# Kernel optimization log

Measured on AMD Instinct MI355X. Metric: run time of the kernel, lower is better.

The kernel has to match this reference:

```python
import jax, jax.numpy as jnp
import numpy as np

NN = 1024  # nodes per LSTM layer (equal across layers, required by gating broadcast)


def setup_inputs() -> dict:
    key = jax.random.key(0)
    ks = jax.random.split(key, 8)
    T, B, V, E = 64, 64, 32000, 512
    ip = 0.3
    inputs = jax.random.normal(ks[0], (T, B, V), dtype=jnp.float32) * 0.1
    embedding_matrix = jax.random.normal(ks[1], (V, E), dtype=jnp.float32) * (ip * np.sqrt(1.0 / V))
    lstm_w0 = jax.random.normal(ks[2], (E + NN, 4 * NN), dtype=jnp.float32) * (ip * np.sqrt(1.0 / (E + NN)))
    lstm_b0 = jnp.zeros((4 * NN,), dtype=jnp.float32)
    lstm_w1 = jax.random.normal(ks[3], (2 * NN, 4 * NN), dtype=jnp.float32) * (ip * np.sqrt(1.0 / (2 * NN)))
    lstm_b1 = jnp.zeros((4 * NN,), dtype=jnp.float32)
    gates_w = jax.random.normal(ks[4], (2 * NN, 2), dtype=jnp.float32) * (ip * np.sqrt(1.0 / (2 * NN)))
    out_w = jax.random.normal(ks[5], (NN, V), dtype=jnp.float32) * (ip * np.sqrt(1.0 / NN))
    out_b = jnp.zeros((V,), dtype=jnp.float32)
    return dict(inputs=inputs, embedding_matrix=embedding_matrix,
                lstm_w0=lstm_w0, lstm_b0=lstm_b0, lstm_w1=lstm_w1, lstm_b1=lstm_b1,
                gates_w=gates_w, out_w=out_w, out_b=out_b)


def _cell(x, h, c, W, b):
    # concat -> matmul -> bias -> split [3*NN sigmoid | NN tanh] -> gate update
    z = jnp.concatenate([x, h], axis=1) @ W + b
    sig = jax.nn.sigmoid(z[:, : 3 * NN])
    g = jnp.tanh(z[:, 3 * NN:])
    f, i, o = sig[:, :NN], sig[:, NN:2 * NN], sig[:, 2 * NN:]
    c_new = f * c + i * g
    h_new = o * jnp.tanh(c_new)
    return h_new, c_new


def _forward(inputs, embedding_matrix, lstm_w0, lstm_b0, lstm_w1, lstm_b1, gates_w, out_w, out_b):
    T, B, V = inputs.shape
    emb = jnp.einsum('tbv,ve->tbe', inputs, embedding_matrix)  # [T,B,E]

    def step(carry, e_t):
        h0, c0, h1, c1 = carry
        h0, c0 = _cell(e_t, h0, c0, lstm_w0, lstm_b0)
        h1, c1 = _cell(h0, h1, c1, lstm_w1, lstm_b1)
        return (h0, c0, h1, c1), (h0, h1)

    zeros = jnp.zeros((B, NN), dtype=inputs.dtype)
    _, (h0s, h1s) = jax.lax.scan(step, (zeros, zeros, zeros, zeros), emb)
    h0_flat = h0s.reshape(T * B, NN)  # concat along time == stacked reshape
    h1_flat = h1s.reshape(T * B, NN)
    full = jnp.concatenate([h0_flat, h1_flat], axis=1)  # [T*B, 2*NN]
    gates = jax.nn.sigmoid(full @ gates_w)               # [T*B, 2]
    gated = gates[:, 0:1] * h0_flat + gates[:, 1:2] * h1_flat
    logits = gated @ out_w + out_b                       # [T*B, V]
    return logits


def reference(inputs, embedding_matrix, lstm_w0, lstm_b0, lstm_w1, lstm_b1, gates_w, out_w, out_b):
    return _forward(inputs, embedding_matrix, lstm_w0, lstm_b0, lstm_w1, lstm_b1, gates_w, out_w, out_b)
```

## Files before the change

kernel.cpp:

```cpp
#include <hip/hip_runtime.h>
#include <math.h>

typedef __attribute__((ext_vector_type(8))) short bf16x8;
typedef __attribute__((ext_vector_type(4))) float f32x4;
typedef __attribute__((ext_vector_type(8))) _Float16 f16x8;
typedef unsigned short ushort_t;

#define T_STEPS 64
#define BATCH   64
#define VOCAB   32000
#define EMB     512
#define HID     1024
#define G4      4096

__device__ __forceinline__ unsigned short f2bf(float x) {
    unsigned u = __builtin_bit_cast(unsigned, x);
    u += 0x7FFFu + ((u >> 16) & 1u);
    return (unsigned short)(u >> 16);
}
__device__ __forceinline__ float bf2f(unsigned short h) {
    unsigned u = ((unsigned)h) << 16;
    return __builtin_bit_cast(float, u);
}
__device__ __forceinline__ unsigned pack2(unsigned short a, unsigned short b) {
    return (unsigned)a | ((unsigned)b << 16);
}
__device__ __forceinline__ unsigned short f2h(float x) {
    return __builtin_bit_cast(unsigned short, (_Float16)x);
}
__device__ __forceinline__ float h2f(unsigned short h) {
    return (float)__builtin_bit_cast(_Float16, h);
}
__device__ __forceinline__ f32x4 ntload4(const float* p) {
    return __builtin_nontemporal_load((const f32x4*)p);
}

__device__ __forceinline__ size_t packA_off(int row, int k, int M16) {
    return ((size_t)((k >> 5) * M16 + (row >> 4))) * 512 +
           ((k & 31) >> 3) * 128 + (row & 15) * 8 + (k & 7);
}

template<int BM, int BN, int NW_M, int NW_N, bool NTA, bool NTC>
__launch_bounds__(NW_M * NW_N * 64)
__global__ void gemm_a32b16(const float* __restrict__ A, const ushort_t* __restrict__ Bp,
                            float* __restrict__ C, int lda, int ldc, int K8,
                            int KCHUNK, size_t chunkStride, float invScale) {
    constexpr int THREADS = NW_M * NW_N * 64;
    constexpr int MF = BM / NW_M / 16;
    constexpr int NF = BN / NW_N / 16;
    __shared__ _Float16 AhS[BM][40];

    const int tid  = threadIdx.x;
    const int row0 = blockIdx.y * BM;
    const int gBase = blockIdx.x * (BN / 16);
    const int kBeg = blockIdx.z * KCHUNK;
    C += (size_t)blockIdx.z * chunkStride;

    const int l = tid & 63, w = tid >> 6;
    const int wm = w / NW_N, wn = w % NW_N;
    const int lr = l & 15, lk = l >> 4;

    f32x4 acc[MF][NF];
#pragma unroll
    for (int m = 0; m < MF; ++m)
#pragma unroll
        for (int n = 0; n < NF; ++n)
#pragma unroll
            for (int r = 0; r < 4; ++r) acc[m][n][r] = 0.f;

    constexpr int AI = BM * 4 / THREADS;

    for (int k0 = 0; k0 < KCHUNK; k0 += 32) {
#pragma unroll
        for (int i = 0; i < AI; ++i) {
            int f = tid + i * THREADS;
            int r = f >> 2, k8 = (f & 3) << 3;
            const float* ap = A + (size_t)(row0 + r) * lda + kBeg + k0 + k8;
            f32x4 v0, v1;
            if (NTA) { v0 = ntload4(ap); v1 = ntload4(ap + 4); }
            else     { v0 = *(const f32x4*)ap; v1 = *(const f32x4*)(ap + 4); }
            f16x8 hv;
            hv[0] = (_Float16)v0[0]; hv[1] = (_Float16)v0[1];
            hv[2] = (_Float16)v0[2]; hv[3] = (_Float16)v0[3];
            hv[4] = (_Float16)v1[0]; hv[5] = (_Float16)v1[1];
            hv[6] = (_Float16)v1[2]; hv[7] = (_Float16)v1[3];
            *(f16x8*)&AhS[r][k8] = hv;
        }
        __syncthreads();
        const size_t kRow = (size_t)((kBeg + k0) >> 3) + lk;
        f16x8 a[MF], b[NF];
#pragma unroll
        for (int n = 0; n < NF; ++n) {
            int g = gBase + wn * NF + n;
            b[n] = *(const f16x8*)(Bp + ((size_t)g * K8 + kRow) * 128 + lr * 8);
        }
#pragma unroll
        for (int m = 0; m < MF; ++m)
            a[m] = *(const f16x8*)&AhS[wm * MF * 16 + m * 16 + lr][lk * 8];
#pragma unroll
        for (int m = 0; m < MF; ++m)
#pragma unroll
            for (int n = 0; n < NF; ++n)
                acc[m][n] = __builtin_amdgcn_mfma_f32_16x16x32_f16(a[m], b[n], acc[m][n], 0, 0, 0);
        __syncthreads();
    }

#pragma unroll
    for (int n = 0; n < NF; ++n) {
        int col = (gBase + wn * NF + n) * 16 + lr;
#pragma unroll
        for (int m = 0; m < MF; ++m) {
            int rbase = row0 + wm * MF * 16 + m * 16 + lk * 4;
#pragma unroll
            for (int r = 0; r < 4; ++r) {
                float v = acc[m][n][r] * invScale;
                float* cp = &C[(size_t)(rbase + r) * ldc + col];
                if (NTC) __builtin_nontemporal_store(v, cp);
                else *cp = v;
            }
        }
    }
}

__global__ void reduce8(const float* __restrict__ zp, float* __restrict__ out, size_t cs) {
    size_t i = ((size_t)blockIdx.x * 256 + threadIdx.x) * 4;
    f32x4 a = *(const f32x4*)(zp + i);
#pragma unroll
    for (int c = 1; c < 8; ++c) {
        f32x4 b = *(const f32x4*)(zp + c * cs + i);
        a += b;
    }
    *(f32x4*)(out + i) = a;
}

template<bool PERM>
__launch_bounds__(256)
__global__ void wcv16(const float* __restrict__ W, ushort_t* __restrict__ Wp,
                      int Krows, int ldW, float scale) {
    __shared__ float tile[32][33];
    const int k0 = blockIdx.x * 32;
    const int n0 = blockIdx.y * 32;
    const int tid = threadIdx.x;
#pragma unroll
    for (int i = 0; i < 4; ++i) {
        int idx = tid + i * 256;
        int r = idx >> 5, c = idx & 31;
        tile[r][c] = W[(size_t)(k0 + r) * ldW + n0 + c];
    }
    __syncthreads();
    const int rn = tid >> 3;
    const int cq = (tid & 7) * 4;
    unsigned short h[4];
#pragma unroll
    for (int j = 0; j < 4; ++j) h[j] = f2h(tile[cq + j][rn] * scale);
    const int n = n0 + rn;
    const int p = PERM ? (((n & 1023) >> 2) * 16 + (n >> 10) * 4 + (n & 3)) : n;
    const int k = k0 + cq;
    size_t off = ((size_t)(p >> 4) * (Krows >> 3) + (k >> 3)) * 128 + (p & 15) * 8 + (k & 7);
    uint2 hp; hp.x = pack2(h[0], h[1]); hp.y = pack2(h[2], h[3]);
    *(uint2*)(Wp + off) = hp;
}

template<int K>
__device__ __forceinline__ void lstm_body(
        float* red, int cg,
        const ushort_t* Ah, const ushort_t* Al,
        const ushort_t* Wp,
        const float* xpart, const float* bias,
        float* c_state, float* histF,
        ushort_t* d1h, ushort_t* d1l,
        ushort_t* d2h, ushort_t* d2l) {
    const int tid = threadIdx.x;
    const int l = tid & 63, w = tid >> 6;
    const int lr = l & 15, lk = l >> 4;
    constexpr int spw = K >> 8;
    const size_t wbase = (size_t)cg * (K >> 3) * 128 + lk * 128 + lr * 8;

    f32x4 acc[4];
#pragma unroll
    for (int m = 0; m < 4; ++m)
#pragma unroll
        for (int r = 0; r < 4; ++r) acc[m][r] = 0.f;

    const int s0 = w * spw;
    const ushort_t* wptr = Wp + wbase + (size_t)s0 * 512;
    const ushort_t* aptr = Ah + (size_t)s0 * 4 * 512 + l * 8;
    const ushort_t* lptr = Al + (size_t)s0 * 4 * 512 + l * 8;
#pragma unroll
    for (int s = 0; s < spw; ++s) {
        f16x8 bw = *(const f16x8*)(wptr + (size_t)s * 512);
#pragma unroll
        for (int m = 0; m < 4; ++m) {
            f16x8 ah = *(const f16x8*)(aptr + (size_t)(s * 4 + m) * 512);
            f16x8 al = *(const f16x8*)(lptr + (size_t)(s * 4 + m) * 512);
            acc[m] = __builtin_amdgcn_mfma_f32_16x16x32_f16(ah, bw, acc[m], 0, 0, 0);
            acc[m] = __builtin_amdgcn_mfma_f32_16x16x32_f16(al, bw, acc[m], 0, 0, 0);
        }
    }
#pragma unroll
    for (int m = 0; m < 4; ++m)
        *(f32x4*)&red[(w * 64 + l) * 20 + m * 4] = acc[m];
    __syncthreads();

    if (tid < 256) {
        const int r = tid >> 2, v = tid & 3;
        const int m = r >> 4, lkq = (r >> 2) & 3, reg = r & 3;
        const int u = cg * 4 + v;
        constexpr float invS = 1.f / 65536.f;
        float z[4];
#pragma unroll
        for (int j = 0; j < 4; ++j) {
            const int c = j * 4 + v;
            float s = 0.f;
#pragma unroll
            for (int ww = 0; ww < 8; ++ww)
                s += red[(ww * 64 + lkq * 16 + c) * 20 + m * 4 + reg];
            s = s * invS + bias[j * 1024 + u];
            if (xpart)
                s += __builtin_nontemporal_load(&xpart[(size_t)r * 4096 + j * 1024 + u]);
            z[j] = s;
        }
        float f = 1.f / (1.f + expf(-z[0]));
        float i = 1.f / (1.f + expf(-z[1]));
        float o = 1.f / (1.f + expf(-z[2]));
        float g = tanhf(z[3]);
        const int cidx = r * 1024 + u;
        float cn = f * c_state[cidx] + i * g;
        c_state[cidx] = cn;
        float hn = o * tanhf(cn);
        __builtin_nontemporal_store(hn, &histF[cidx]);
        float hs = hn * 256.f;
        unsigned short hh = f2h(hs);
        unsigned short hl = f2h(hs - h2f(hh));
        size_t o1 = packA_off(r, u, 4);
        d1h[o1] = hh; d1l[o1] = hl;
        if (d2h) {
            size_t o2 = packA_off(r, u, 4);
            d2h[o2] = hh; d2l[o2] = hl;
        }
    }
    __syncthreads();
}

__launch_bounds__(512)
__global__ void lstm_pair(int active0, int active1,
        const ushort_t* Ah0, const ushort_t* Al0, const ushort_t* Wp0,
        const float* xpart0, const float* bias0,
        float* c0, float* hist0,
        ushort_t* d1h0, ushort_t* d1l0, ushort_t* d2h0, ushort_t* d2l0,
        const ushort_t* Ah1, const ushort_t* Al1, const ushort_t* Wp1,
        const float* bias1, float* c1, float* hist1,
        ushort_t* d1h1, ushort_t* d1l1) {
    __shared__ float red[512 * 20];
    const int b = blockIdx.x;
    if (b < 256) {
        if (!active0) return;
        lstm_body<1024>(red, b, Ah0, Al0, Wp0, xpart0, bias0,
                        c0, hist0, d1h0, d1l0, d2h0, d2l0);
    } else {
        if (!active1) return;
        lstm_body<2048>(red, b - 256, Ah1, Al1, Wp1, nullptr, bias1,
                        c1, hist1, d1h1, d1l1, nullptr, nullptr);
    }
}

__launch_bounds__(256)
__global__ void gates_gated(const float* __restrict__ h0s, const float* __restrict__ h1s,
                            const float* __restrict__ gw,
                            ushort_t* __restrict__ gA16) {
    const int r = blockIdx.x;
    const int tid = threadIdx.x;
    const float* h0r = h0s + (size_t)r * HID;
    const float* h1r = h1s + (size_t)r * HID;
    float p0 = 0.f, p1 = 0.f;
    for (int k = tid; k < HID; k += 256) {
        float v0 = h0r[k], v1 = h1r[k];
        p0 += v0 * gw[2 * k]     + v1 * gw[2 * (HID + k)];
        p1 += v0 * gw[2 * k + 1] + v1 * gw[2 * (HID + k) + 1];
    }
#pragma unroll
    for (int off = 32; off; off >>= 1) {
        p0 += __shfl_down(p0, off);
        p1 += __shfl_down(p1, off);
    }
    __shared__ float s0[4], s1[4];
    __shared__ float gg[2];
    if ((tid & 63) == 0) { s0[tid >> 6] = p0; s1[tid >> 6] = p1; }
    __syncthreads();
    if (tid == 0) {
        float a = s0[0] + s0[1] + s0[2] + s0[3];
        float b = s1[0] + s1[1] + s1[2] + s1[3];
        gg[0] = 1.f / (1.f + expf(-a));
        gg[1] = 1.f / (1.f + expf(-b));
    }
    __syncthreads();
    float g0 = gg[0], g1 = gg[1];
    const int n0 = tid * 4;
    unsigned short h[4];
#pragma unroll
    for (int j = 0; j < 4; ++j) {
        int n = n0 + j;
        h[j] = f2h((g0 * h0r[n] + g1 * h1r[n]) * 256.f);
    }
    uint2 hp; hp.x = pack2(h[0], h[1]); hp.y = pack2(h[2], h[3]);
    *(uint2*)(gA16 + packA_off(r, n0, 256)) = hp;
}

__launch_bounds__(512)
__global__ void gemm_out_v4(const ushort_t* __restrict__ gA16, const ushort_t* __restrict__ Bp,
                            const float* __restrict__ bias, float* __restrict__ C) {
    __shared__ ushort_t AL[2][8192];
    __shared__ ushort_t BL[2][4096];

    const int tid = threadIdx.x;
    const int lin = (blockIdx.x & 7) * 500 + (blockIdx.x >> 3);
    const int bi = lin / 250, bj = lin % 250;
    const int row0 = bi * 256, col0 = bj * 128;

    const int l = tid & 63, w = tid >> 6;
    const int wm = w >> 1, wn = w & 1;
    const int lr = l & 15, lk = l >> 4;

    const int aOff = tid * 8;
    const size_t bBase = (size_t)(bj * 8 + (tid >> 6)) * 16384 + (tid & 63) * 8;

    f32x4 acc[4][4];
#pragma unroll
    for (int m = 0; m < 4; ++m)
#pragma unroll
        for (int n = 0; n < 4; ++n)
#pragma unroll
            for (int r = 0; r < 4; ++r) acc[m][n][r] = 0.f;

    {
        const size_t cA = ((size_t)(bi * 16)) * 512;
        uint4 a0 = *(const uint4*)(gA16 + cA + aOff);
        uint4 a1 = *(const uint4*)(gA16 + cA + 4096 + aOff);
        uint4 b0 = *(const uint4*)(Bp + bBase);
        *(uint4*)&AL[0][aOff] = a0;
        *(uint4*)&AL[0][4096 + aOff] = a1;
        *(uint4*)&BL[0][aOff & 4095] = b0;
    }
    __syncthreads();

    uint4 rA0, rA1, rB;
    for (int k32 = 0; k32 < 32; ++k32) {
        const int cur = k32 & 1, nxt = cur ^ 1;
        const bool hasNext = (k32 < 31);
        if (hasNext) {
            const size_t cA = ((size_t)((k32 + 1) * 256 + bi * 16)) * 512;
            rA0 = *(const uint4*)(gA16 + cA + aOff);
            rA1 = *(const uint4*)(gA16 + cA + 4096 + aOff);
            rB  = *(const uint4*)(Bp + bBase + (size_t)(k32 + 1) * 512);
        }
        f16x8 a[4], b[4];
#pragma unroll
        for (int m = 0; m < 4; ++m)
            a[m] = *(const f16x8*)&AL[cur][(wm * 4 + m) * 512 + l * 8];
#pragma unroll
        for (int n = 0; n < 4; ++n)
            b[n] = *(const f16x8*)&BL[cur][(wn * 4 + n) * 512 + l * 8];
#pragma unroll
        for (int m = 0; m < 4; ++m)
#pragma unroll
            for (int n = 0; n < 4; ++n)
                acc[m][n] = __builtin_amdgcn_mfma_f32_16x16x32_f16(a[m], b[n], acc[m][n], 0, 0, 0);
        if (hasNext) {
            *(uint4*)&AL[nxt][aOff] = rA0;
            *(uint4*)&AL[nxt][4096 + aOff] = rA1;
            *(uint4*)&BL[nxt][aOff & 4095] = rB;
        }
        __syncthreads();
    }

    constexpr float invScale = 1.f / 65536.f;
#pragma unroll
    for (int n = 0; n < 4; ++n) {
        int col = col0 + wn * 64 + n * 16 + lr;
        float bv = bias[col];
#pragma unroll
        for (int m = 0; m < 4; ++m) {
            int rbase = row0 + wm * 64 + m * 16 + lk * 4;
#pragma unroll
            for (int r = 0; r < 4; ++r)
                __builtin_nontemporal_store(acc[m][n][r] * invScale + bv,
                                            &C[(size_t)(rbase + r) * VOCAB + col]);
        }
    }
}

extern "C" void kernel_launch(void* const* d_in, const int* in_sizes, int n_in,
                              void* d_out, int out_size, void* d_ws, size_t ws_size,
                              hipStream_t stream) {
    const float* inputs = (const float*)d_in[0];
    const float* embm   = (const float*)d_in[1];
    const float* w0     = (const float*)d_in[2];
    const float* b0     = (const float*)d_in[3];
    const float* w1     = (const float*)d_in[4];
    const float* b1     = (const float*)d_in[5];
    const float* gw     = (const float*)d_in[6];
    const float* outw   = (const float*)d_in[7];
    const float* outb   = (const float*)d_in[8];
    float* logits = (float*)d_out;

    float* ws    = (float*)d_ws;
    float* emb   = ws;
    float* h0s   = ws + 2097152;
    float* h1s   = ws + 6291456;
    ushort_t* gA16 = (ushort_t*)(ws + 10485760);
    float* c0    = ws + 14942208;
    float* c1    = ws + 15007744;
    ushort_t* hpB = (ushort_t*)(ws + 15073280);
    ushort_t* outw16 = (ushort_t*)(ws + 15466496);

    ushort_t* hp0h[2] = { hpB,            hpB + 65536 };
    ushort_t* hp0l[2] = { hpB + 131072,   hpB + 196608 };
    ushort_t* hp1h[2] = { hpB + 262144,   hpB + 393216 };
    ushort_t* hp1l[2] = { hpB + 524288,   hpB + 655360 };

    float* zpEmb = (float*)d_out;
    float* z0x   = (float*)d_out + 16777216;
    ushort_t* wt0 = (ushort_t*)((float*)d_out + 33554432);
    ushort_t* wt1 = wt0 + 4194304;
    ushort_t* embm16 = wt1 + 8388608;
    ushort_t* w0x16  = embm16 + 16384000;

    (void)hipMemsetAsync(c0, 0, (size_t)524288 * sizeof(float), stream);

    wcv16<false><<<dim3(1000, 16), 256, 0, stream>>>(embm, embm16, VOCAB, EMB, 256.f);
    wcv16<false><<<dim3(16, 128), 256, 0, stream>>>(w0, w0x16, EMB, G4, 256.f);
    wcv16<false><<<dim3(32, 1000), 256, 0, stream>>>(outw, outw16, HID, VOCAB, 256.f);
    wcv16<true><<<dim3(32, 128), 256, 0, stream>>>(w0 + (size_t)512 * G4, wt0, 1024, G4, 256.f);
    wcv16<true><<<dim3(64, 128), 256, 0, stream>>>(w1, wt1, 2048, G4, 256.f);

    gemm_a32b16<128, 512, 2, 4, true, false><<<dim3(1, 32, 8), 512, 0, stream>>>(
        inputs, embm16, zpEmb, VOCAB, EMB, VOCAB / 8, VOCAB / 8, (size_t)4096 * EMB, 1.f / 256.f);
    reduce8<<<2048, 256, 0, stream>>>(zpEmb, emb, (size_t)4096 * EMB);

    gemm_a32b16<128, 128, 2, 2, false, true><<<dim3(32, 32, 1), 256, 0, stream>>>(
        emb, w0x16, z0x, EMB, G4, EMB / 8, EMB, 0, 1.f / 256.f);

    for (int t = 0; t <= T_STEPS; ++t) {
        const int p0 = t & 1, q0 = (t + 1) & 1;
        const int s  = t - 1, ss = s < 0 ? 0 : s;
        const int p1 = ss & 1, q1 = (ss + 1) & 1;
        lstm_pair<<<512, 512, 0, stream>>>(
            (t < T_STEPS) ? 1 : 0, (t >= 1) ? 1 : 0,
            hp0h[p0], hp0l[p0], wt0,
            z0x + (size_t)(t < T_STEPS ? t : 0) * 262144, b0,
            c0, h0s + (size_t)(t < T_STEPS ? t : 0) * 65536,
            hp0h[q0], hp0l[q0], hp1h[p0], hp1l[p0],
            hp1h[p1], hp1l[p1], wt1,
            b1, c1, h1s + (size_t)ss * 65536,
            hp1h[q1] + 65536, hp1l[q1] + 65536);
    }

    gates_gated<<<4096, 256, 0, stream>>>(h0s, h1s, gw, gA16);

    gemm_out_v4<<<4000, 512, 0, stream>>>(gA16, outw16, outb, logits);
}
```

Before: 1.810 ms.

## Add software-pipelined embedding GEMM and two-stage-prefetch output GEMM

Replaces the generic split-K embedding GEMM with a dedicated kernel that double-buffers fp32-to-fp16 converted A tiles in shared memory and keeps B fragments in registers. Global loads for step k+2 are issued before the MFMAs of step k. The output GEMM loop is unrolled into a ping-pong form with two register sets, so loads run two steps ahead of compute. The aim is to hide global memory latency behind MFMA work, at the cost of higher register pressure and a hand-coded K-loop tail.

Result: no change. 1.776 ms (-1.9%).

```diff
diff --git a/kernel.cpp b/kernel.cpp
--- a/kernel.cpp
+++ b/kernel.cpp
@@ -38,6 +38,100 @@
 __device__ __forceinline__ size_t packA_off(int row, int k, int M16) {
     return ((size_t)((k >> 5) * M16 + (row >> 4))) * 512 +
            ((k & 31) >> 3) * 128 + (row & 15) * 8 + (k & 7);
+}
+
+__launch_bounds__(512, 2)
+__global__ void gemm_emb(const float* __restrict__ A, const ushort_t* __restrict__ Bp,
+                         float* __restrict__ C) {
+    __shared__ _Float16 AhS[2][128][40];
+    const int tid = threadIdx.x;
+    const int row0 = blockIdx.x * 128;
+    const int z = blockIdx.y;
+    const int kBeg = z * 4000;
+    const int kb8  = z * 500;
+    C += (size_t)z * 4096 * EMB;
+
+    const int l = tid & 63, w = tid >> 6;
+    const int wm = w >> 2, wn = w & 3;
+    const int lr = l & 15, lk = l >> 4;
+
+    const int ar = tid >> 2, ak8 = (tid & 3) << 3;
+    const float* Abase = A + (size_t)(row0 + ar) * VOCAB + kBeg + ak8;
+
+    f32x4 acc[4][8];
+#pragma unroll
+    for (int m = 0; m < 4; ++m)
+#pragma unroll
+        for (int n = 0; n < 8; ++n)
+#pragma unroll
+            for (int r = 0; r < 4; ++r) acc[m][n][r] = 0.f;
+
+    auto loadB = [&](int k, f16x8* dst) {
+#pragma unroll
+        for (int n = 0; n < 8; ++n) {
+            int g = wn * 8 + n;
+            dst[n] = *(const f16x8*)(Bp + ((size_t)g * 4000 + kb8 + k * 4 + lk) * 128 + lr * 8);
+        }
+    };
+    auto loadA = [&](int k, f32x4& v0, f32x4& v1) {
+        const float* ap = Abase + k * 32;
+        v0 = ntload4(ap); v1 = ntload4(ap + 4);
+    };
+    auto storeA = [&](int buf, f32x4 v0, f32x4 v1) {
+        f16x8 hv;
+        hv[0] = (_Float16)v0[0]; hv[1] = (_Float16)v0[1];
+        hv[2] = (_Float16)v0[2]; hv[3] = (_Float16)v0[3];
+        hv[4] = (_Float16)v1[0]; hv[5] = (_Float16)v1[1];
+        hv[6] = (_Float16)v1[2]; hv[7] = (_Float16)v1[3];
+        *(f16x8*)&AhS[buf][ar][ak8] = hv;
+    };
+    auto mfmaStep = [&](int buf, f16x8* bset) {
+        f16x8 a[4];
+#pragma unroll
+        for (int m = 0; m < 4; ++m)
+            a[m] = *(const f16x8*)&AhS[buf][wm * 64 + m * 16 + lr][lk * 8];
+#pragma unroll
+        for (int m = 0; m < 4; ++m)
+#pragma unroll
+            for (int n = 0; n < 8; ++n)
+                acc[m][n] = __builtin_amdgcn_mfma_f32_16x16x32_f16(a[m], bset[n], acc[m][n], 0, 0, 0);
+    };
+
+    f16x8 bA[8], bB[8];
+    f32x4 a0A, a1A, a0B, a1B;
+    {
+        f32x4 t0, t1;
+        loadA(0, t0, t1); storeA(0, t0, t1);
+        loadA(1, a0A, a1A);
+        loadB(0, bA); loadB(1, bB);
+        __syncthreads();
+    }
+    for (int k = 0; k < 124; k += 2) {
+        if (k + 2 < 125) loadA(k + 2, a0B, a1B);
+        mfmaStep(0, bA);
+        if (k + 2 < 125) loadB(k + 2, bA);
+        storeA(1, a0A, a1A);
+        __syncthreads();
+        if (k + 3 < 125) loadA(k + 3, a0A, a1A);
+        mfmaStep(1, bB);
+        if (k + 3 < 125) loadB(k + 3, bB);
+        if (k + 2 < 125) storeA(0, a0B, a1B);
+        __syncthreads();
+    }
+    mfmaStep(0, bA);
+
+    constexpr float invScale = 1.f / 256.f;
+#pragma unroll
+    for (int n = 0; n < 8; ++n) {
+        int col = (wn * 8 + n) * 16 + lr;
+#pragma unroll
+        for (int m = 0; m < 4; ++m) {
+            int rbase = row0 + wm * 64 + m * 16 + lk * 4;
+#pragma unroll
+            for (int r = 0; r < 4; ++r)
+                C[(size_t)(rbase + r) * EMB + col] = acc[m][n][r] * invScale;
+        }
+    }
 }
 
 template<int BM, int BN, int NW_M, int NW_N, bool NTA, bool NTC>
@@ -307,7 +401,7 @@
 }
 
 __launch_bounds__(512)
-__global__ void gemm_out_v4(const ushort_t* __restrict__ gA16, const ushort_t* __restrict__ Bp,
+__global__ void gemm_out_v5(const ushort_t* __restrict__ gA16, const ushort_t* __restrict__ Bp,
                             const float* __restrict__ bias, float* __restrict__ C) {
     __shared__ ushort_t AL[2][8192];
     __shared__ ushort_t BL[2][4096];
@@ -332,43 +426,48 @@
 #pragma unroll
             for (int r = 0; r < 4; ++r) acc[m][n][r] = 0.f;
 
-    {
-        const size_t cA = ((size_t)(bi * 16)) * 512;
-        uint4 a0 = *(const uint4*)(gA16 + cA + aOff);
-        uint4 a1 = *(const uint4*)(gA16 + cA + 4096 + aOff);
-        uint4 b0 = *(const uint4*)(Bp + bBase);
-        *(uint4*)&AL[0][aOff] = a0;
-        *(uint4*)&AL[0][4096 + aOff] = a1;
-        *(uint4*)&BL[0][aOff & 4095] = b0;
-    }
-    __syncthreads();
-
-    uint4 rA0, rA1, rB;
-    for (int k32 = 0; k32 < 32; ++k32) {
-        const int cur = k32 & 1, nxt = cur ^ 1;
-        const bool hasNext = (k32 < 31);
-        if (hasNext) {
-            const size_t cA = ((size_t)((k32 + 1) * 256 + bi * 16)) * 512;
-            rA0 = *(const uint4*)(gA16 + cA + aOff);
-            rA1 = *(const uint4*)(gA16 + cA + 4096 + aOff);
-            rB  = *(const uint4*)(Bp + bBase + (size_t)(k32 + 1) * 512);
-        }
+    auto LA0 = [&](int k) { return *(const uint4*)(gA16 + ((size_t)(k * 256 + bi * 16)) * 512 + aOff); };
+    auto LA1 = [&](int k) { return *(const uint4*)(gA16 + ((size_t)(k * 256 + bi * 16)) * 512 + 4096 + aOff); };
+    auto LB  = [&](int k) { return *(const uint4*)(Bp + bBase + (size_t)k * 512); };
+    auto MF  = [&](int buf) {
         f16x8 a[4], b[4];
 #pragma unroll
         for (int m = 0; m < 4; ++m)
-            a[m] = *(const f16x8*)&AL[cur][(wm * 4 + m) * 512 + l * 8];
+            a[m] = *(const f16x8*)&AL[buf][(wm * 4 + m) * 512 + l * 8];
 #pragma unroll
         for (int n = 0; n < 4; ++n)
-            b[n] = *(const f16x8*)&BL[cur][(wn * 4 + n) * 512 + l * 8];
+            b[n] = *(const f16x8*)&BL[buf][(wn * 4 + n) * 512 + l * 8];
 #pragma unroll
         for (int m = 0; m < 4; ++m)
 #pragma unroll
             for (int n = 0; n < 4; ++n)
                 acc[m][n] = __builtin_amdgcn_mfma_f32_16x16x32_f16(a[m], b[n], acc[m][n], 0, 0, 0);
-        if (hasNext) {
-            *(uint4*)&AL[nxt][aOff] = rA0;
-            *(uint4*)&AL[nxt][4096 + aOff] = rA1;
-            *(uint4*)&BL[nxt][aOff & 4095] = rB;
+    };
+
+    {
+        uint4 t0 = LA0(0), t1 = LA1(0), t2 = LB(0);
+        *(uint4*)&AL[0][aOff] = t0;
+        *(uint4*)&AL[0][4096 + aOff] = t1;
+        *(uint4*)&BL[0][aOff & 4095] = t2;
+    }
+    uint4 pA0 = LA0(1), pA1 = LA1(1), pB = LB(1);
+    uint4 qA0 = {}, qA1 = {}, qB = {};
+    __syncthreads();
+
+#pragma unroll
+    for (int k = 0; k < 32; k += 2) {
+        if (k + 2 < 32) { qA0 = LA0(k + 2); qA1 = LA1(k + 2); qB = LB(k + 2); }
+        MF(0);
+        *(uint4*)&AL[1][aOff] = pA0;
+        *(uint4*)&AL[1][4096 + aOff] = pA1;
+        *(uint4*)&BL[1][aOff & 4095] = pB;
+        __syncthreads();
+        if (k + 3 < 32) { pA0 = LA0(k + 3); pA1 = LA1(k + 3); pB = LB(k + 3); }
+        MF(1);
+        if (k + 2 < 32) {
+            *(uint4*)&AL[0][aOff] = qA0;
+            *(uint4*)&AL[0][4096 + aOff] = qA1;
+            *(uint4*)&BL[0][aOff & 4095] = qB;
         }
         __syncthreads();
     }
@@ -433,8 +532,7 @@
     wcv16<true><<<dim3(32, 128), 256, 0, stream>>>(w0 + (size_t)512 * G4, wt0, 1024, G4, 256.f);
     wcv16<true><<<dim3(64, 128), 256, 0, stream>>>(w1, wt1, 2048, G4, 256.f);
 
-    gemm_a32b16<128, 512, 2, 4, true, false><<<dim3(1, 32, 8), 512, 0, stream>>>(
-        inputs, embm16, zpEmb, VOCAB, EMB, VOCAB / 8, VOCAB / 8, (size_t)4096 * EMB, 1.f / 256.f);
+    gemm_emb<<<dim3(32, 8), 512, 0, stream>>>(inputs, embm16, zpEmb);
     reduce8<<<2048, 256, 0, stream>>>(zpEmb, emb, (size_t)4096 * EMB);
 
     gemm_a32b16<128, 128, 2, 2, false, true><<<dim3(32, 32, 1), 256, 0, stream>>>(
@@ -457,5 +555,5 @@
 
     gates_gated<<<4096, 256, 0, stream>>>(h0s, h1s, gw, gA16);
 
-    gemm_out_v4<<<4000, 512, 0, stream>>>(gA16, outw16, outb, logits);
-}
+    gemm_out_v5<<<4000, 512, 0, stream>>>(gA16, outw16, outb, logits);
+}
```
